# Kernel tuning notes

Hardware: AMD Instinct MI355X
Metric: run time of the kernel (lower is better)

The kernel has to match this reference:

```python
import jax, jax.numpy as jnp
import numpy as np

EMBED_DIM = 1024
NUM_HEADS = 16
HEAD_DIM = EMBED_DIM // NUM_HEADS
SCALE = HEAD_DIM ** -0.5
BATCH, SEQ = 4, 2048


def setup_inputs() -> dict:
    key = jax.random.key(0)
    ks = jax.random.split(key, 9)
    s = EMBED_DIM ** -0.5
    return {
        "query": jax.random.normal(ks[0], (BATCH, SEQ, EMBED_DIM), jnp.float32),
        "Wq": jax.random.normal(ks[1], (EMBED_DIM, EMBED_DIM), jnp.float32) * s,
        "bq": jax.random.normal(ks[2], (EMBED_DIM,), jnp.float32) * 0.02,
        "Wk": jax.random.normal(ks[3], (EMBED_DIM, EMBED_DIM), jnp.float32) * s,
        "bk": jax.random.normal(ks[4], (EMBED_DIM,), jnp.float32) * 0.02,
        "Wv": jax.random.normal(ks[5], (EMBED_DIM, EMBED_DIM), jnp.float32) * s,
        "bv": jax.random.normal(ks[6], (EMBED_DIM,), jnp.float32) * 0.02,
        "Wo": jax.random.normal(ks[7], (EMBED_DIM, EMBED_DIM), jnp.float32) * s,
        "bo": jax.random.normal(ks[8], (EMBED_DIM,), jnp.float32) * 0.02,
    }


def reference(query, Wq, bq, Wk, bk, Wv, bv, Wo, bo):
    B, T, E = query.shape
    H, D = NUM_HEADS, HEAD_DIM
    # projections (torch Linear: x @ W.T + b); key=value=query (self-attention)
    q = (query @ Wq.T + bq).reshape(B, T, H, D).transpose(0, 2, 1, 3)  # [B,H,T,D]
    k = (query @ Wk.T + bk).reshape(B, T, H, D).transpose(0, 2, 1, 3)
    v = (query @ Wv.T + bv).reshape(B, T, H, D).transpose(0, 2, 1, 3)
    scores = jnp.einsum("bhtd,bhsd->bhts", q, k) * SCALE  # [B,H,T,T]
    probs = jax.nn.softmax(scores, axis=-1)
    ctx = jnp.einsum("bhts,bhsd->bhtd", probs, v)  # [B,H,T,D]
    ctx = ctx.transpose(0, 2, 1, 3).reshape(B, T, E)
    out = ctx @ Wo.T + bo
    return out
```

## Files before the change

kernel.cpp:

```cpp
#include <hip/hip_runtime.h>
#include <cstdint>

#define DEV __device__ __forceinline__

using short8   = __attribute__((ext_vector_type(8))) short;
using floatx4  = __attribute__((ext_vector_type(4))) float;
using ushortx4 = __attribute__((ext_vector_type(4))) unsigned short;
using intx4    = __attribute__((ext_vector_type(4))) int;

#define MFMA_BF16(a, b, c) __builtin_amdgcn_mfma_f32_16x16x32_bf16((a), (b), (c), 0, 0, 0)

static constexpr float QK_SCALE_LOG2E = 0.18033688011112042f;

DEV unsigned short f2bf(float f) {
  unsigned int u = __builtin_bit_cast(unsigned int, f);
  u += 0x7FFFu + ((u >> 16) & 1u);
  return (unsigned short)(u >> 16);
}

DEV int cvt_pk_bf16(float lo, float hi) {
  int r;
  asm("v_cvt_pk_bf16_f32 %0, %1, %2" : "=v"(r) : "v"(lo), "v"(hi));
  return r;
}

DEV void gload_lds16(const void* g, void* l) {
  __builtin_amdgcn_global_load_lds(
      (const __attribute__((address_space(1))) void*)g,
      (__attribute__((address_space(3))) void*)l, 16, 0, 0);
}

__global__ void cvt_f32_bf16(const float* __restrict__ src,
                             unsigned short* __restrict__ dst, int n4) {
  int i = blockIdx.x * blockDim.x + threadIdx.x;
  if (i >= n4) return;
  float4 v = reinterpret_cast<const float4*>(src)[i];
  ushortx4 o = {f2bf(v.x), f2bf(v.y), f2bf(v.z), f2bf(v.w)};
  reinterpret_cast<ushortx4*>(dst)[i] = o;
}

__global__ void cvt_w4(const float* __restrict__ w0, const float* __restrict__ w1,
                       const float* __restrict__ w2, const float* __restrict__ w3,
                       unsigned short* __restrict__ dst) {
  int i = blockIdx.x * blockDim.x + threadIdx.x;
  int b = i >> 18;
  const float* src = (b == 0) ? w0 : (b == 1) ? w1 : (b == 2) ? w2 : w3;
  int off = i & 0x3FFFF;
  float4 v = reinterpret_cast<const float4*>(src)[off];
  ushortx4 o = {f2bf(v.x), f2bf(v.y), f2bf(v.z), f2bf(v.w)};
  reinterpret_cast<ushortx4*>(dst)[i] = o;
}

DEV void stage128x64(const unsigned short* gbase, int ld, unsigned short* lds, int tid) {
#pragma unroll
  for (int j = 0; j < 4; ++j) {
    int s = j * 256 + tid;
    int row = s >> 3, slot = s & 7;
    int chunk = slot ^ (row & 7);
    gload_lds16(gbase + row * ld + chunk * 8, (char*)lds + s * 16);
  }
}

template <int KMODE>
DEV void stage64x64_8w(const unsigned short* gbase, int ld, unsigned short* lds, int tid) {
  int row = tid >> 3, slot = tid & 7;
  int mask = KMODE ? ((row & 3) | ((row >> 1) & 4)) : (row & 7);
  int chunk = slot ^ mask;
  gload_lds16(gbase + row * ld + chunk * 8, (char*)lds + tid * 16);
}

__global__ __launch_bounds__(256, 2) void gemm_qkv(
    const unsigned short* __restrict__ A,
    const unsigned short* __restrict__ Wqkv,
    const float* __restrict__ bq, const float* __restrict__ bk,
    const float* __restrict__ bv,
    unsigned short* __restrict__ Qb, unsigned short* __restrict__ Kb,
    unsigned short* __restrict__ Vtb) {
  __shared__ __attribute__((aligned(16))) unsigned short As[128 * 64];
  __shared__ __attribute__((aligned(16))) unsigned short Bs[128 * 64];
  const int tid = threadIdx.x;
  const int wv = tid >> 6, lane = tid & 63;
  const int g = lane >> 4, rc = lane & 15;
  const int wr = wv >> 1, wc = wv & 1;
  const int nt = blockIdx.x >> 3;
  const int n0 = (blockIdx.x & 7) * 128;
  const int m0 = blockIdx.y * 128;
  const float* bias = (nt == 0) ? bq : (nt == 1) ? bk : bv;

  floatx4 acc[4][4] = {};
  const unsigned short* Ag = A + (size_t)m0 * 1024;
  const unsigned short* Wg = Wqkv + ((size_t)nt << 20) + (size_t)n0 * 1024;

  for (int kt = 0; kt < 16; ++kt) {
    stage128x64(Ag + kt * 64, 1024, As, tid);
    stage128x64(Wg + kt * 64, 1024, Bs, tid);
    __syncthreads();
    short8 af[4][2], bf[4][2];
#pragma unroll
    for (int m = 0; m < 4; ++m)
#pragma unroll
      for (int kk = 0; kk < 2; ++kk) {
        int row = wr * 64 + m * 16 + rc;
        int slot = (kk * 4 + g) ^ (row & 7);
        af[m][kk] = *reinterpret_cast<const short8*>(As + row * 64 + slot * 8);
      }
#pragma unroll
    for (int n = 0; n < 4; ++n)
#pragma unroll
      for (int kk = 0; kk < 2; ++kk) {
        int row = wc * 64 + n * 16 + rc;
        int slot = (kk * 4 + g) ^ (row & 7);
        bf[n][kk] = *reinterpret_cast<const short8*>(Bs + row * 64 + slot * 8);
      }
#pragma unroll
    for (int m = 0; m < 4; ++m)
#pragma unroll
      for (int n = 0; n < 4; ++n) {
        acc[m][n] = MFMA_BF16(af[m][0], bf[n][0], acc[m][n]);
        acc[m][n] = MFMA_BF16(af[m][1], bf[n][1], acc[m][n]);
      }
    __syncthreads();
  }

#pragma unroll
  for (int m = 0; m < 4; ++m) {
    const int gm = m0 + wr * 64 + m * 16 + g * 4;
#pragma unroll
    for (int n = 0; n < 4; ++n) {
      const int gn = n0 + wc * 64 + n * 16 + rc;
      const float bs = bias[gn];
      floatx4 v = acc[m][n];
      if (nt == 2) {
        const int bb = gm >> 11, t0 = gm & 2047;
        const int hh = gn >> 6, dd = gn & 63;
        ushortx4 p = {f2bf(v[0] + bs), f2bf(v[1] + bs), f2bf(v[2] + bs), f2bf(v[3] + bs)};
        *reinterpret_cast<ushortx4*>(Vtb + ((size_t)((bb * 16 + hh) * 64 + dd)) * 2048 + t0) = p;
      } else {
        unsigned short* O = (nt == 0) ? Qb : Kb;
        const float sc = (nt == 0) ? QK_SCALE_LOG2E : 1.0f;
#pragma unroll
        for (int i = 0; i < 4; ++i)
          O[(size_t)(gm + i) * 1024 + gn] = f2bf((v[i] + bs) * sc);
      }
    }
  }
}

__global__ __launch_bounds__(256, 2) void gemm_out(
    const unsigned short* __restrict__ A,
    const unsigned short* __restrict__ W,
    const float* __restrict__ bias,
    float* __restrict__ out) {
  __shared__ __attribute__((aligned(16))) unsigned short As[128 * 64];
  __shared__ __attribute__((aligned(16))) unsigned short Bs[128 * 64];
  const int tid = threadIdx.x;
  const int wv = tid >> 6, lane = tid & 63;
  const int g = lane >> 4, rc = lane & 15;
  const int wr = wv >> 1, wc = wv & 1;
  const int m0 = blockIdx.y * 128, n0 = blockIdx.x * 128;

  floatx4 acc[4][4] = {};
  const unsigned short* Ag = A + (size_t)m0 * 1024;
  const unsigned short* Wg = W + (size_t)n0 * 1024;

  for (int kt = 0; kt < 16; ++kt) {
    stage128x64(Ag + kt * 64, 1024, As, tid);
    stage128x64(Wg + kt * 64, 1024, Bs, tid);
    __syncthreads();
    short8 af[4][2], bf[4][2];
#pragma unroll
    for (int m = 0; m < 4; ++m)
#pragma unroll
      for (int kk = 0; kk < 2; ++kk) {
        int row = wr * 64 + m * 16 + rc;
        int slot = (kk * 4 + g) ^ (row & 7);
        af[m][kk] = *reinterpret_cast<const short8*>(As + row * 64 + slot * 8);
      }
#pragma unroll
    for (int n = 0; n < 4; ++n)
#pragma unroll
      for (int kk = 0; kk < 2; ++kk) {
        int row = wc * 64 + n * 16 + rc;
        int slot = (kk * 4 + g) ^ (row & 7);
        bf[n][kk] = *reinterpret_cast<const short8*>(Bs + row * 64 + slot * 8);
      }
#pragma unroll
    for (int m = 0; m < 4; ++m)
#pragma unroll
      for (int n = 0; n < 4; ++n) {
        acc[m][n] = MFMA_BF16(af[m][0], bf[n][0], acc[m][n]);
        acc[m][n] = MFMA_BF16(af[m][1], bf[n][1], acc[m][n]);
      }
    __syncthreads();
  }

#pragma unroll
  for (int m = 0; m < 4; ++m) {
    const int gm = m0 + wr * 64 + m * 16 + g * 4;
#pragma unroll
    for (int n = 0; n < 4; ++n) {
      const int gn = n0 + wc * 64 + n * 16 + rc;
      const float bs = bias[gn];
#pragma unroll
      for (int i = 0; i < 4; ++i) out[(size_t)(gm + i) * 1024 + gn] = acc[m][n][i] + bs;
    }
  }
}

__global__ __launch_bounds__(512, 4) void attn_fwd(
    const unsigned short* __restrict__ Q,
    const unsigned short* __restrict__ K,
    const unsigned short* __restrict__ Vt,
    unsigned short* __restrict__ ctx) {
  __shared__ __attribute__((aligned(16))) unsigned short Ks0[64 * 64];
  __shared__ __attribute__((aligned(16))) unsigned short Ks1[64 * 64];
  __shared__ __attribute__((aligned(16))) unsigned short Vs0[64 * 64];
  __shared__ __attribute__((aligned(16))) unsigned short Vs1[64 * 64];
  const int tid = threadIdx.x;
  const int wv = tid >> 6, lane = tid & 63;
  const int g = lane >> 4, rc = lane & 15;
  const int f = blockIdx.x;
  const int i_ = f >> 3;
  const int bh = (f & 7) * 8 + (i_ & 7);
  const int qb = i_ >> 3;
  const int b = bh >> 4, h = bh & 15;
  const int q0 = qb * 256 + wv * 32;

  short8 qfr[2][2];
  {
    const unsigned short* Qg = Q + (size_t)(b * 2048 + q0 + rc) * 1024 + h * 64 + g * 8;
#pragma unroll
    for (int q_ = 0; q_ < 2; ++q_)
#pragma unroll
      for (int kk = 0; kk < 2; ++kk)
        qfr[q_][kk] = *reinterpret_cast<const short8*>(Qg + q_ * 16 * 1024 + kk * 32);
  }

  const unsigned short* Kg = K + (size_t)b * 2048 * 1024 + h * 64;
  const unsigned short* Vg = Vt + (size_t)bh * 64 * 2048;

  const int i4 = rc & 3, g4 = rc >> 2;
  const int kmask = i4 | ((g4 & 1) << 2);
  const int koff0 = ((g4 * 8 + i4) * 64 + ((g)     ^ kmask) * 8) * 2;
  const int koff1 = ((g4 * 8 + i4) * 64 + ((4 + g) ^ kmask) * 8) * 2;
  const int vmask = rc & 7;
  const int voff0 = (rc * 64 + ((g)     ^ vmask) * 8) * 2;
  const int voff1 = (rc * 64 + ((4 + g) ^ vmask) * 8) * 2;

  const int one2 = 0x3F803F80;
  intx4 ones_i = (rc == 0) ? intx4{one2, one2, one2, one2} : intx4{0, 0, 0, 0};
  const short8 vf_ones = __builtin_bit_cast(short8, ones_i);

  floatx4 acc[2][4] = {};
  floatx4 acc5[2] = {};

  auto tile_compute = [&](const unsigned short* KsB, const unsigned short* VsB) {
    floatx4 sv[2][4] = {};
    __builtin_amdgcn_s_setprio(1);
#pragma unroll
    for (int nf = 0; nf < 4; ++nf) {
      const int ro = ((nf >> 1) * 32 + (nf & 1) * 4) * 128;
      short8 kf0 = *reinterpret_cast<const short8*>((const char*)KsB + ro + koff0);
      short8 kf1 = *reinterpret_cast<const short8*>((const char*)KsB + ro + koff1);
      sv[0][nf] = MFMA_BF16(kf0, qfr[0][0], sv[0][nf]);
      sv[0][nf] = MFMA_BF16(kf1, qfr[0][1], sv[0][nf]);
      sv[1][nf] = MFMA_BF16(kf0, qfr[1][0], sv[1][nf]);
      sv[1][nf] = MFMA_BF16(kf1, qfr[1][1], sv[1][nf]);
    }
    __builtin_amdgcn_s_setprio(0);

#pragma unroll
    for (int q_ = 0; q_ < 2; ++q_)
#pragma unroll
      for (int nf = 0; nf < 4; ++nf)
#pragma unroll
        for (int i = 0; i < 4; ++i)
          sv[q_][nf][i] = __builtin_amdgcn_exp2f(sv[q_][nf][i]);

#pragma unroll
    for (int kb = 0; kb < 2; ++kb) {
      intx4 w0, w1;
#pragma unroll
      for (int w = 0; w < 4; ++w) {
        const int nf = 2 * kb + (w >> 1), ii = (w & 1) * 2;
        w0[w] = cvt_pk_bf16(sv[0][nf][ii], sv[0][nf][ii + 1]);
        w1[w] = cvt_pk_bf16(sv[1][nf][ii], sv[1][nf][ii + 1]);
      }
      short8 pb0 = __builtin_bit_cast(short8, w0);
      short8 pb1 = __builtin_bit_cast(short8, w1);
      const int vo = kb ? voff1 : voff0;
      __builtin_amdgcn_s_setprio(1);
#pragma unroll
      for (int nd = 0; nd < 4; ++nd) {
        short8 vf = *reinterpret_cast<const short8*>((const char*)VsB + nd * 2048 + vo);
        acc[0][nd] = MFMA_BF16(vf, pb0, acc[0][nd]);
        acc[1][nd] = MFMA_BF16(vf, pb1, acc[1][nd]);
      }
      acc5[0] = MFMA_BF16(vf_ones, pb0, acc5[0]);
      acc5[1] = MFMA_BF16(vf_ones, pb1, acc5[1]);
      __builtin_amdgcn_s_setprio(0);
    }
  };

  stage64x64_8w<1>(Kg, 1024, Ks0, tid);
  stage64x64_8w<0>(Vg, 2048, Vs0, tid);
  __syncthreads();

  for (int t = 0; t < 32; t += 2) {
    stage64x64_8w<1>(Kg + (size_t)(t + 1) * 64 * 1024, 1024, Ks1, tid);
    stage64x64_8w<0>(Vg + (t + 1) * 64, 2048, Vs1, tid);
    tile_compute(Ks0, Vs0);
    __syncthreads();
    if (t + 2 < 32) {
      stage64x64_8w<1>(Kg + (size_t)(t + 2) * 64 * 1024, 1024, Ks0, tid);
      stage64x64_8w<0>(Vg + (t + 2) * 64, 2048, Vs0, tid);
    }
    tile_compute(Ks1, Vs1);
    __syncthreads();
  }

#pragma unroll
  for (int q_ = 0; q_ < 2; ++q_) {
    const float l = __shfl(acc5[q_][0], rc);
    const float inv = 1.0f / l;
    unsigned short* Cp = ctx + (size_t)(b * 2048 + q0 + q_ * 16 + rc) * 1024 + h * 64 + g * 4;
#pragma unroll
    for (int nd = 0; nd < 4; ++nd) {
      ushortx4 o = {f2bf(acc[q_][nd][0] * inv), f2bf(acc[q_][nd][1] * inv),
                    f2bf(acc[q_][nd][2] * inv), f2bf(acc[q_][nd][3] * inv)};
      *reinterpret_cast<ushortx4*>(Cp + nd * 16) = o;
    }
  }
}

extern "C" void kernel_launch(void* const* d_in, const int* in_sizes, int n_in,
                              void* d_out, int out_size, void* d_ws, size_t ws_size,
                              hipStream_t stream) {
  (void)in_sizes; (void)n_in; (void)out_size; (void)ws_size;
  const float* x  = (const float*)d_in[0];
  const float* Wq = (const float*)d_in[1];
  const float* bq = (const float*)d_in[2];
  const float* Wk = (const float*)d_in[3];
  const float* bk = (const float*)d_in[4];
  const float* Wv = (const float*)d_in[5];
  const float* bv = (const float*)d_in[6];
  const float* Wo = (const float*)d_in[7];
  const float* bo = (const float*)d_in[8];

  unsigned short* Xb  = (unsigned short*)d_ws;
  unsigned short* Wqb = Xb + (size_t)8192 * 1024;
  unsigned short* Wob = Wqb + (size_t)3 * 1024 * 1024;
  unsigned short* Vtb = Wob + (size_t)1024 * 1024;
  unsigned short* Ctx = Xb;
  unsigned short* Qb = (unsigned short*)d_out;
  unsigned short* Kb = Qb + (size_t)8192 * 1024;

  cvt_f32_bf16<<<8192, 256, 0, stream>>>(x, Xb, 8192 * 1024 / 4);
  cvt_w4<<<4096, 256, 0, stream>>>(Wq, Wk, Wv, Wo, Wqb);

  gemm_qkv<<<dim3(24, 64), 256, 0, stream>>>(Xb, Wqb, bq, bk, bv, Qb, Kb, Vtb);
  attn_fwd<<<512, 512, 0, stream>>>(Qb, Kb, Vtb, Ctx);
  gemm_out<<<dim3(8, 64), 256, 0, stream>>>(Ctx, Wob, bo, (float*)d_out);
}
```

Before: 158.1 us.

## Fuse input conversion kernels and remap GEMM tiles for XCD-local L2 reuse

Merges the activation and weight fp32-to-bf16 conversion kernels into one launch, removing one kernel launch and its tail. Changes both GEMMs to a 1D grid and remaps the block index so that blocks landing on the same XCD (round-robin by id&7) share the same group of M rows. This keeps A-tile reuse inside each XCD's L2. The risk is that weight tiles are now spread across all XCDs, and the mapping assumes round-robin block dispatch over 8 XCDs.

```diff
diff --git a/kernel.cpp b/kernel.cpp
--- a/kernel.cpp
+++ b/kernel.cpp
@@ -30,25 +30,25 @@
       (__attribute__((address_space(3))) void*)l, 16, 0, 0);
 }
 
-__global__ void cvt_f32_bf16(const float* __restrict__ src,
-                             unsigned short* __restrict__ dst, int n4) {
+__global__ void cvt_all(const float* __restrict__ x,
+                        const float* __restrict__ w0, const float* __restrict__ w1,
+                        const float* __restrict__ w2, const float* __restrict__ w3,
+                        unsigned short* __restrict__ Xb,
+                        unsigned short* __restrict__ Wb) {
   int i = blockIdx.x * blockDim.x + threadIdx.x;
-  if (i >= n4) return;
-  float4 v = reinterpret_cast<const float4*>(src)[i];
-  ushortx4 o = {f2bf(v.x), f2bf(v.y), f2bf(v.z), f2bf(v.w)};
-  reinterpret_cast<ushortx4*>(dst)[i] = o;
-}
-
-__global__ void cvt_w4(const float* __restrict__ w0, const float* __restrict__ w1,
-                       const float* __restrict__ w2, const float* __restrict__ w3,
-                       unsigned short* __restrict__ dst) {
-  int i = blockIdx.x * blockDim.x + threadIdx.x;
-  int b = i >> 18;
-  const float* src = (b == 0) ? w0 : (b == 1) ? w1 : (b == 2) ? w2 : w3;
-  int off = i & 0x3FFFF;
-  float4 v = reinterpret_cast<const float4*>(src)[off];
-  ushortx4 o = {f2bf(v.x), f2bf(v.y), f2bf(v.z), f2bf(v.w)};
-  reinterpret_cast<ushortx4*>(dst)[i] = o;
+  if (i < 2097152) {
+    float4 v = reinterpret_cast<const float4*>(x)[i];
+    ushortx4 o = {f2bf(v.x), f2bf(v.y), f2bf(v.z), f2bf(v.w)};
+    reinterpret_cast<ushortx4*>(Xb)[i] = o;
+  } else {
+    int j = i - 2097152;
+    int b = j >> 18;
+    const float* src = (b == 0) ? w0 : (b == 1) ? w1 : (b == 2) ? w2 : w3;
+    int off = j & 0x3FFFF;
+    float4 v = reinterpret_cast<const float4*>(src)[off];
+    ushortx4 o = {f2bf(v.x), f2bf(v.y), f2bf(v.z), f2bf(v.w)};
+    reinterpret_cast<ushortx4*>(Wb)[j] = o;
+  }
 }
 
 DEV void stage128x64(const unsigned short* gbase, int ld, unsigned short* lds, int tid) {
@@ -82,9 +82,12 @@
   const int wv = tid >> 6, lane = tid & 63;
   const int g = lane >> 4, rc = lane & 15;
   const int wr = wv >> 1, wc = wv & 1;
-  const int nt = blockIdx.x >> 3;
-  const int n0 = (blockIdx.x & 7) * 128;
-  const int m0 = blockIdx.y * 128;
+  const int id = blockIdx.x;
+  const int xcd = id & 7, c = id >> 3;
+  const int mloc = c & 7, ng = c >> 3;
+  const int nt = ng >> 3;
+  const int n0 = (ng & 7) * 128;
+  const int m0 = (xcd * 8 + mloc) * 128;
   const float* bias = (nt == 0) ? bq : (nt == 1) ? bk : bv;
 
   floatx4 acc[4][4] = {};
@@ -157,7 +160,11 @@
   const int wv = tid >> 6, lane = tid & 63;
   const int g = lane >> 4, rc = lane & 15;
   const int wr = wv >> 1, wc = wv & 1;
-  const int m0 = blockIdx.y * 128, n0 = blockIdx.x * 128;
+  const int id = blockIdx.x;
+  const int xcd = id & 7, c = id >> 3;
+  const int mloc = c & 7, nx = c >> 3;
+  const int m0 = (xcd * 8 + mloc) * 128;
+  const int n0 = nx * 128;
 
   floatx4 acc[4][4] = {};
   const unsigned short* Ag = A + (size_t)m0 * 1024;
@@ -355,10 +362,9 @@
   unsigned short* Qb = (unsigned short*)d_out;
   unsigned short* Kb = Qb + (size_t)8192 * 1024;
 
-  cvt_f32_bf16<<<8192, 256, 0, stream>>>(x, Xb, 8192 * 1024 / 4);
-  cvt_w4<<<4096, 256, 0, stream>>>(Wq, Wk, Wv, Wo, Wqb);
-
-  gemm_qkv<<<dim3(24, 64), 256, 0, stream>>>(Xb, Wqb, bq, bk, bv, Qb, Kb, Vtb);
+  cvt_all<<<12288, 256, 0, stream>>>(x, Wq, Wk, Wv, Wo, Xb, Wqb);
+
+  gemm_qkv<<<1536, 256, 0, stream>>>(Xb, Wqb, bq, bk, bv, Qb, Kb, Vtb);
   attn_fwd<<<512, 512, 0, stream>>>(Qb, Kb, Vtb, Ctx);
-  gemm_out<<<dim3(8, 64), 256, 0, stream>>>(Ctx, Wob, bo, (float*)d_out);
-}
+  gemm_out<<<512, 256, 0, stream>>>(Ctx, Wob, bo, (float*)d_out);
+}
```

Measured after the change: 151.2 us. 4.4% less time.
